# Kernel optimization log

Measured on AMD Instinct MI355X. Metric: run time of the kernel, lower is better.

## Reference

```python
import jax, jax.numpy as jnp
import numpy as np

T, D, H, E, K = 8192, 1024, 768, 16, 2


def setup_inputs() -> dict:
    key = jax.random.key(0)
    k1, k2, k3, k4, k5, k6 = jax.random.split(key, 6)
    x = jax.random.normal(k1, (T, D), dtype=jnp.float32)
    weights = jax.random.uniform(k2, (T, K), dtype=jnp.float32)
    indices = jax.random.randint(k3, (T, K), 0, E, dtype=jnp.int64)
    counts = jax.random.randint(k4, (E,), 0, 1024, dtype=jnp.int32)
    # GatedMLP params per expert: fc1: D -> 2H (value | gate), fc2: H -> D, no bias
    W1 = jax.random.normal(k5, (E, D, 2 * H), dtype=jnp.float32) * (1.0 / np.sqrt(D))
    W2 = jax.random.normal(k6, (E, H, D), dtype=jnp.float32) * (1.0 / np.sqrt(H))
    return {"x": x, "weights": weights, "indices": indices, "counts": counts, "W1": W1, "W2": W2}


def _gated_mlp(x, w1, w2):
    h = x @ w1                      # [T, 2H]
    v, g = jnp.split(h, 2, axis=-1)  # value, gate halves (torch chunk order)
    return (v * jax.nn.silu(g)) @ w2  # [T, D]


def reference(x, weights, indices, counts, W1, W2):
    # y[t] = sum_k weights[t,k] * GatedMLP_{indices[t,k]}(x[t])
    # Expressed as a masked per-expert combine: w_e[t] = sum_k weights[t,k]*[indices[t,k]==e].
    # Identical math to the torch gather/scatter loop (zero weight -> zero contribution).
    n_experts = W1.shape[0]
    y = jnp.zeros_like(x)
    for e in range(n_experts):
        w_e = jnp.sum(weights * (indices == e), axis=-1)  # [T]
        y = y + _gated_mlp(x, W1[e], W2[e]) * w_e[:, None]
    return y
```

## Files before the change

kernel.cpp:

```cpp
#include <hip/hip_runtime.h>
#include <hip/hip_bf16.h>

#define T_TOK 8192
#define D_DIM 1024
#define H_DIM 768
#define E_EXP 16
#define K_TOP 2
#define TK (T_TOK * K_TOP)
#define NT128 144

typedef __bf16 bf16x8 __attribute__((ext_vector_type(8)));
typedef unsigned short u16x8 __attribute__((ext_vector_type(8)));
typedef float f32x4 __attribute__((ext_vector_type(4)));

typedef const __attribute__((address_space(1))) void* gas_t;
typedef __attribute__((address_space(3))) void* las_t;

__device__ __forceinline__ unsigned short f2b(float f) {
    __hip_bfloat16 h = __float2bfloat16(f);
    return __builtin_bit_cast(unsigned short, h);
}
__device__ __forceinline__ float b2f(unsigned short u) {
    unsigned int x = ((unsigned int)u) << 16;
    return __builtin_bit_cast(float, x);
}

__global__ __launch_bounds__(1024) void k_route(
    const int* __restrict__ idx, const float* __restrict__ wts,
    int* __restrict__ offs, int* __restrict__ tiletab,
    int* __restrict__ rows, float* __restrict__ wslot, int* __restrict__ slot_of) {
    __shared__ int lcnt[E_EXP];
    __shared__ int lcur[E_EXP];
    const int tid = threadIdx.x;
    if (tid < E_EXP) lcnt[tid] = 0;
    __syncthreads();
    for (int i = tid; i < TK; i += 1024) atomicAdd(&lcnt[idx[i]], 1);
    __syncthreads();
    if (tid == 0) {
        int s = 0, nt = 0;
        for (int e = 0; e < E_EXP; ++e) {
            offs[e] = s;
            lcur[e] = s;
            const int n = lcnt[e];
            for (int m0 = 0; m0 < n; m0 += 128) tiletab[nt++] = (e << 16) | (m0 >> 7);
            s += n;
        }
        offs[E_EXP] = s;
        for (int i = nt; i < NT128; ++i) tiletab[i] = -1;
    }
    __syncthreads();
    for (int i = tid; i < TK; i += 1024) {
        const int e = idx[i];
        const int p = atomicAdd(&lcur[e], 1);
        rows[p] = i >> 1;
        wslot[p] = wts[i];
        slot_of[i] = p;
    }
}

#define PRB_X 2048
#define PRB_W1 3072
#define PRB_W2 1536
#define PRB_TOT (1 + PRB_X + PRB_W1 + PRB_W2)

__global__ __launch_bounds__(512) void k_preproute(
    const float* __restrict__ x, const float* __restrict__ W1, const float* __restrict__ W2,
    const int* __restrict__ idx, const float* __restrict__ wts,
    unsigned short* __restrict__ xb, unsigned short* __restrict__ W1T,
    unsigned short* __restrict__ W2T,
    int* __restrict__ offs, int* __restrict__ tiletab,
    int* __restrict__ rows, float* __restrict__ wslot, int* __restrict__ slot_of) {
    const int b = blockIdx.x;
    const int tid = threadIdx.x;
    if (b == 0) {
        __shared__ int lcnt[E_EXP];
        __shared__ int lcur[E_EXP];
        if (tid < E_EXP) lcnt[tid] = 0;
        __syncthreads();
        for (int i = tid; i < TK; i += 512) atomicAdd(&lcnt[idx[i]], 1);
        __syncthreads();
        if (tid == 0) {
            int s = 0, nt = 0;
            for (int e = 0; e < E_EXP; ++e) {
                offs[e] = s;
                lcur[e] = s;
                const int n = lcnt[e];
                for (int m0 = 0; m0 < n; m0 += 128) tiletab[nt++] = (e << 16) | (m0 >> 7);
                s += n;
            }
            offs[E_EXP] = s;
            for (int i = nt; i < NT128; ++i) tiletab[i] = -1;
        }
        __syncthreads();
        for (int i = tid; i < TK; i += 512) {
            const int e = idx[i];
            const int p = atomicAdd(&lcur[e], 1);
            rows[p] = i >> 1;
            wslot[p] = wts[i];
            slot_of[i] = p;
        }
        return;
    }
    if (b <= PRB_X) {
        const size_t base = (size_t)(b - 1) * 4096 + (size_t)tid * 8;
        const float4 v0 = *reinterpret_cast<const float4*>(&x[base]);
        const float4 v1 = *reinterpret_cast<const float4*>(&x[base + 4]);
        u16x8 u;
        u[0] = f2b(v0.x); u[1] = f2b(v0.y); u[2] = f2b(v0.z); u[3] = f2b(v0.w);
        u[4] = f2b(v1.x); u[5] = f2b(v1.y); u[6] = f2b(v1.z); u[7] = f2b(v1.w);
        *reinterpret_cast<u16x8*>(&xb[base]) = u;
        return;
    }
    __shared__ float t4[2][64][65];
    const int sub = tid >> 8, t2 = tid & 255;
    const float* src; unsigned short* dst;
    int K, C, e, kb, cb, pack;
    if (b <= PRB_X + PRB_W1) {
        const int q = (b - 1 - PRB_X) * 2 + sub;
        K = D_DIM; C = 2 * H_DIM; pack = 1;
        e = q / 384; const int r = q % 384;
        kb = (r % 16) * 64; cb = (r / 16) * 64;
        src = W1; dst = W1T;
    } else {
        const int q = (b - 1 - PRB_X - PRB_W1) * 2 + sub;
        K = H_DIM; C = D_DIM; pack = 0;
        e = q / 192; const int r = q % 192;
        kb = (r % 12) * 64; cb = (r / 12) * 64;
        src = W2; dst = W2T;
    }
    const float* s = src + ((size_t)e * K + kb) * C + cb;
#pragma unroll
    for (int i = 0; i < 4; ++i) {
        const int kk = (t2 >> 4) + i * 16, c4 = (t2 & 15) * 4;
        const float4 v = *reinterpret_cast<const float4*>(&s[(size_t)kk * C + c4]);
        t4[sub][kk][c4] = v.x; t4[sub][kk][c4 + 1] = v.y;
        t4[sub][kk][c4 + 2] = v.z; t4[sub][kk][c4 + 3] = v.w;
    }
    __syncthreads();
#pragma unroll
    for (int i = 0; i < 2; ++i) {
        const int cc = (t2 >> 3) + i * 32, k8 = (t2 & 7) * 8;
        const int j = cb + cc;
        int drow;
        if (pack) drow = (j < H_DIM) ? ((j >> 5) * 64 + (j & 31))
                                     : (((j - H_DIM) >> 5) * 64 + 32 + ((j - H_DIM) & 31));
        else drow = j;
        u16x8 u;
#pragma unroll
        for (int q8 = 0; q8 < 8; ++q8) u[q8] = f2b(t4[sub][k8 + q8][cc]);
        *reinterpret_cast<u16x8*>(&dst[((size_t)e * C + drow) * K + kb + k8]) = u;
    }
}


__global__ __launch_bounds__(512, 2) void k_gemm1_fast(
    const unsigned short* __restrict__ xb, const unsigned short* __restrict__ W1T,
    const int* __restrict__ offs, const int* __restrict__ tiletab,
    const int* __restrict__ rows, unsigned short* __restrict__ act) {
    const int ti = (blockIdx.x & 7) * (NT128 / 8) + (blockIdx.x >> 3);
    const int tt = tiletab[ti];
    if (tt < 0) return;
    const int e = tt >> 16, m0 = (tt & 0xffff) << 7;
    const int off = offs[e], n_e = offs[e + 1] - off;
    const int by = blockIdx.y;

    __shared__ unsigned short SA[2][128 * 32];
    __shared__ unsigned short SB[2][256 * 32];

    const int tid = threadIdx.x;
    const int wid = tid >> 6, lane = tid & 63;
    const int l15 = lane & 15, kq = lane >> 4;
    const int wm = wid >> 2, wn = wid & 3;
    const int srow = tid >> 2;
    const int esw = (((tid & 3) ^ ((tid >> 3) & 3)) << 3);
    const int rk = ((kq ^ ((l15 >> 1) & 3)) << 3);

    int tok;
    { int s = m0 + srow; s = (s < n_e) ? s : (n_e - 1); tok = rows[off + s]; }
    size_t bB[2];
#pragma unroll
    for (int j = 0; j < 2; ++j)
        bB[j] = ((size_t)e * (2 * H_DIM) + by * 256 + j * 128 + srow) * D_DIM + esw;

    f32x4 acc[4][4];
#pragma unroll
    for (int m = 0; m < 4; ++m)
#pragma unroll
        for (int n = 0; n < 4; ++n)
#pragma unroll
            for (int r = 0; r < 4; ++r) acc[m][n][r] = 0.f;

    auto stage = [&](int buf, int k0) {
        const unsigned short* ga = xb + (size_t)tok * D_DIM + k0 + esw;
        __builtin_amdgcn_global_load_lds((gas_t)ga,
            (las_t)((char*)&SA[buf][0] + tid * 16), 16, 0, 0);
#pragma unroll
        for (int j = 0; j < 2; ++j) {
            const unsigned short* gb = W1T + bB[j] + k0;
            __builtin_amdgcn_global_load_lds((gas_t)gb,
                (las_t)((char*)&SB[buf][0] + j * 8192 + tid * 16), 16, 0, 0);
        }
    };

    stage(0, 0);
    stage(1, 32);
    int c = 0;
    const int NT = D_DIM / 32;
    for (int t = 0; t < NT; ++t) {
        if (t < NT - 1) asm volatile("s_waitcnt vmcnt(3)" ::: "memory");
        else            asm volatile("s_waitcnt vmcnt(0)" ::: "memory");
        __builtin_amdgcn_s_barrier();
        asm volatile("" ::: "memory");
        bf16x8 a[4], b[4];
#pragma unroll
        for (int m = 0; m < 4; ++m) {
            const int row = wm * 64 + m * 16 + l15;
            a[m] = __builtin_bit_cast(bf16x8, *reinterpret_cast<const u16x8*>(
                &SA[c][row * 32 + rk]));
        }
#pragma unroll
        for (int n = 0; n < 4; ++n) {
            const int row = wn * 64 + n * 16 + l15;
            b[n] = __builtin_bit_cast(bf16x8, *reinterpret_cast<const u16x8*>(
                &SB[c][row * 32 + rk]));
        }
#pragma unroll
        for (int m = 0; m < 4; ++m)
#pragma unroll
            for (int n = 0; n < 4; ++n)
                acc[m][n] = __builtin_amdgcn_mfma_f32_16x16x32_bf16(a[m], b[n], acc[m][n], 0, 0, 0);
        asm volatile("s_waitcnt lgkmcnt(0)" ::: "memory");
        __builtin_amdgcn_s_barrier();
        asm volatile("" ::: "memory");
        if (t + 2 < NT) stage(c, (t + 2) * 32);
        c ^= 1;
    }
#pragma unroll
    for (int m = 0; m < 4; ++m)
#pragma unroll
        for (int r = 0; r < 4; ++r) {
            const int row = wm * 64 + m * 16 + kq * 4 + r;
            if (m0 + row < n_e) {
#pragma unroll
                for (int nv = 0; nv < 2; ++nv) {
                    const int col = by * 128 + wn * 32 + nv * 16 + l15;
                    const float vv = acc[m][nv][r], gg = acc[m][2 + nv][r];
                    const float s = gg / (1.0f + __expf(-gg));
                    act[(size_t)(off + m0 + row) * H_DIM + col] = f2b(vv * s);
                }
            }
        }
}

__global__ __launch_bounds__(512, 2) void k_gemm2_fast(
    const unsigned short* __restrict__ act, const unsigned short* __restrict__ W2T,
    const int* __restrict__ offs, const int* __restrict__ tiletab,
    const float* __restrict__ wslot, unsigned short* __restrict__ slot_out) {
    const int ti = (blockIdx.x & 7) * (NT128 / 8) + (blockIdx.x >> 3);
    const int tt = tiletab[ti];
    if (tt < 0) return;
    const int e = tt >> 16, m0 = (tt & 0xffff) << 7;
    const int off = offs[e], n_e = offs[e + 1] - off;
    const int by = blockIdx.y;

    __shared__ unsigned short SA[2][128 * 32];
    __shared__ unsigned short SB[2][256 * 32];

    const int tid = threadIdx.x;
    const int wid = tid >> 6, lane = tid & 63;
    const int l15 = lane & 15, kq = lane >> 4;
    const int wm = wid >> 2, wn = wid & 3;
    const int srow = tid >> 2;
    const int esw = (((tid & 3) ^ ((tid >> 3) & 3)) << 3);
    const int rk = ((kq ^ ((l15 >> 1) & 3)) << 3);

    int slotA;
    { int s = m0 + srow; s = (s < n_e) ? s : (n_e - 1); slotA = off + s; }
    size_t bB[2];
#pragma unroll
    for (int j = 0; j < 2; ++j)
        bB[j] = ((size_t)e * D_DIM + by * 256 + j * 128 + srow) * H_DIM + esw;

    f32x4 acc[4][4];
#pragma unroll
    for (int m = 0; m < 4; ++m)
#pragma unroll
        for (int n = 0; n < 4; ++n)
#pragma unroll
            for (int r = 0; r < 4; ++r) acc[m][n][r] = 0.f;

    auto stage = [&](int buf, int k0) {
        const unsigned short* ga = act + (size_t)slotA * H_DIM + k0 + esw;
        __builtin_amdgcn_global_load_lds((gas_t)ga,
            (las_t)((char*)&SA[buf][0] + tid * 16), 16, 0, 0);
#pragma unroll
        for (int j = 0; j < 2; ++j) {
            const unsigned short* gb = W2T + bB[j] + k0;
            __builtin_amdgcn_global_load_lds((gas_t)gb,
                (las_t)((char*)&SB[buf][0] + j * 8192 + tid * 16), 16, 0, 0);
        }
    };

    stage(0, 0);
    stage(1, 32);
    int c = 0;
    const int NT = H_DIM / 32;
    for (int t = 0; t < NT; ++t) {
        if (t < NT - 1) asm volatile("s_waitcnt vmcnt(3)" ::: "memory");
        else            asm volatile("s_waitcnt vmcnt(0)" ::: "memory");
        __builtin_amdgcn_s_barrier();
        asm volatile("" ::: "memory");
        bf16x8 a[4], b[4];
#pragma unroll
        for (int m = 0; m < 4; ++m) {
            const int row = wm * 64 + m * 16 + l15;
            a[m] = __builtin_bit_cast(bf16x8, *reinterpret_cast<const u16x8*>(
                &SA[c][row * 32 + rk]));
        }
#pragma unroll
        for (int n = 0; n < 4; ++n) {
            const int row = wn * 64 + n * 16 + l15;
            b[n] = __builtin_bit_cast(bf16x8, *reinterpret_cast<const u16x8*>(
                &SB[c][row * 32 + rk]));
        }
#pragma unroll
        for (int m = 0; m < 4; ++m)
#pragma unroll
            for (int n = 0; n < 4; ++n)
                acc[m][n] = __builtin_amdgcn_mfma_f32_16x16x32_bf16(a[m], b[n], acc[m][n], 0, 0, 0);
        asm volatile("s_waitcnt lgkmcnt(0)" ::: "memory");
        __builtin_amdgcn_s_barrier();
        asm volatile("" ::: "memory");
        if (t + 2 < NT) stage(c, (t + 2) * 32);
        c ^= 1;
    }
#pragma unroll
    for (int m = 0; m < 4; ++m)
#pragma unroll
        for (int r = 0; r < 4; ++r) {
            const int row = wm * 64 + m * 16 + kq * 4 + r;
            if (m0 + row < n_e) {
                const int slot = off + m0 + row;
                const float w = wslot[slot];
#pragma unroll
                for (int n = 0; n < 4; ++n) {
                    const int col = by * 256 + wn * 64 + n * 16 + l15;
                    slot_out[(size_t)slot * D_DIM + col] = f2b(w * acc[m][n][r]);
                }
            }
        }
}

__global__ __launch_bounds__(256) void k_gather(const float* __restrict__ x,
                                                const int* __restrict__ rows,
                                                unsigned short* __restrict__ xg) {
    const int s = blockIdx.x, t = threadIdx.x;
    const int tok = rows[s];
    const float4 v = *reinterpret_cast<const float4*>(&x[(size_t)tok * D_DIM + t * 4]);
    ushort4 u;
    u.x = f2b(v.x); u.y = f2b(v.y); u.z = f2b(v.z); u.w = f2b(v.w);
    *reinterpret_cast<ushort4*>(&xg[(size_t)s * D_DIM + t * 4]) = u;
}

__global__ __launch_bounds__(256) void k_gemm1_fb(
    const unsigned short* __restrict__ xg, const float* __restrict__ W1,
    const int* __restrict__ offs, const int* __restrict__ tiletab,
    unsigned short* __restrict__ act) {
    const int tt = tiletab[blockIdx.x];
    if (tt < 0) return;
    const int e = tt >> 16, m0 = (tt & 0xffff) << 7;
    const int off = offs[e], n_e = offs[e + 1] - off;
    const int h0 = blockIdx.y * 64;

    __shared__ unsigned short Ab[128 * 64];
    __shared__ unsigned short Bb[128 * 66];

    const int tid = threadIdx.x;
    const int wid = tid >> 6, lane = tid & 63;
    const int l15 = lane & 15, kq = lane >> 4;

    f32x4 acc[2][8];
#pragma unroll
    for (int m = 0; m < 2; ++m)
#pragma unroll
        for (int n = 0; n < 8; ++n)
#pragma unroll
            for (int r = 0; r < 4; ++r) acc[m][n][r] = 0.f;

    for (int k0 = 0; k0 < D_DIM; k0 += 64) {
        __syncthreads();
#pragma unroll
        for (int j = 0; j < 4; ++j) {
            const int o = wid * 4096 + j * 1024 + lane * 16;
            const int row = o >> 7, kb = o & 127;
            int gr = off + m0 + row; gr = (gr < TK) ? gr : (TK - 1);
            const unsigned short* gp = xg + (size_t)gr * D_DIM + k0 + (kb >> 1);
            __builtin_amdgcn_global_load_lds((gas_t)gp,
                (las_t)((char*)Ab + wid * 4096 + j * 1024), 16, 0, 0);
        }
        {
            const float* W1e = W1 + (size_t)e * D_DIM * (2 * H_DIM);
#pragma unroll
            for (int i = 0; i < 8; ++i) {
                const int flat = tid + 256 * i;
                const int cg = flat & 31, kk = flat >> 5;
                const int cc = cg * 4;
                const int gc = (cc < 64) ? (h0 + cc) : (H_DIM + h0 + cc - 64);
                const float4 v = *reinterpret_cast<const float4*>(
                    &W1e[(size_t)(k0 + kk) * (2 * H_DIM) + gc]);
                Bb[(cc + 0) * 66 + kk] = f2b(v.x);
                Bb[(cc + 1) * 66 + kk] = f2b(v.y);
                Bb[(cc + 2) * 66 + kk] = f2b(v.z);
                Bb[(cc + 3) * 66 + kk] = f2b(v.w);
            }
        }
        __syncthreads();
#pragma unroll
        for (int ks = 0; ks < 2; ++ks) {
            bf16x8 a[2], b[8];
#pragma unroll
            for (int m = 0; m < 2; ++m)
                a[m] = __builtin_bit_cast(bf16x8, *reinterpret_cast<const u16x8*>(
                    &Ab[(wid * 32 + m * 16 + l15) * 64 + ks * 32 + kq * 8]));
#pragma unroll
            for (int n = 0; n < 8; ++n)
                b[n] = __builtin_bit_cast(bf16x8, *reinterpret_cast<const u16x8*>(
                    &Bb[(n * 16 + l15) * 66 + ks * 32 + kq * 8]));
#pragma unroll
            for (int m = 0; m < 2; ++m)
#pragma unroll
                for (int n = 0; n < 8; ++n)
                    acc[m][n] = __builtin_amdgcn_mfma_f32_16x16x32_bf16(a[m], b[n], acc[m][n], 0, 0, 0);
        }
    }
#pragma unroll
    for (int m = 0; m < 2; ++m)
#pragma unroll
        for (int n = 0; n < 4; ++n)
#pragma unroll
            for (int r = 0; r < 4; ++r) {
                const int row = wid * 32 + m * 16 + kq * 4 + r;
                if (m0 + row < n_e) {
                    const float vv = acc[m][n][r], gg = acc[m][n + 4][r];
                    const float s = gg / (1.0f + __expf(-gg));
                    act[(size_t)(off + m0 + row) * H_DIM + h0 + n * 16 + l15] = f2b(vv * s);
                }
            }
}

__global__ __launch_bounds__(256) void k_gemm2_fb(
    const unsigned short* __restrict__ act, const float* __restrict__ W2,
    const int* __restrict__ offs, const int* __restrict__ tiletab,
    const float* __restrict__ wslot, unsigned short* __restrict__ slot_out,
    float* __restrict__ y, const int* __restrict__ rows, int atomic_mode) {
    const int tt = tiletab[blockIdx.x];
    if (tt < 0) return;
    const int e = tt >> 16, m0 = (tt & 0xffff) << 7;
    const int off = offs[e], n_e = offs[e + 1] - off;
    const int n0 = blockIdx.y * 64;

    __shared__ unsigned short Ab[128 * 64];
    __shared__ unsigned short Bb[64 * 66];

    const int tid = threadIdx.x;
    const int wid = tid >> 6, lane = tid & 63;
    const int l15 = lane & 15, kq = lane >> 4;

    f32x4 acc[2][4];
#pragma unroll
    for (int m = 0; m < 2; ++m)
#pragma unroll
        for (int n = 0; n < 4; ++n)
#pragma unroll
            for (int r = 0; r < 4; ++r) acc[m][n][r] = 0.f;

    for (int k0 = 0; k0 < H_DIM; k0 += 64) {
        __syncthreads();
#pragma unroll
        for (int j = 0; j < 4; ++j) {
            const int o = wid * 4096 + j * 1024 + lane * 16;
            const int row = o >> 7, kb = o & 127;
            int gr = off + m0 + row; gr = (gr < TK) ? gr : (TK - 1);
            const unsigned short* gp = act + (size_t)gr * H_DIM + k0 + (kb >> 1);
            __builtin_amdgcn_global_load_lds((gas_t)gp,
                (las_t)((char*)Ab + wid * 4096 + j * 1024), 16, 0, 0);
        }
        {
            const float* W2e = W2 + (size_t)e * H_DIM * D_DIM;
#pragma unroll
            for (int i = 0; i < 4; ++i) {
                const int flat = tid + 256 * i;
                const int cg = flat & 15, kk = flat >> 4;
                const int cc = cg * 4;
                const float4 v = *reinterpret_cast<const float4*>(
                    &W2e[(size_t)(k0 + kk) * D_DIM + n0 + cc]);
                Bb[(cc + 0) * 66 + kk] = f2b(v.x);
                Bb[(cc + 1) * 66 + kk] = f2b(v.y);
                Bb[(cc + 2) * 66 + kk] = f2b(v.z);
                Bb[(cc + 3) * 66 + kk] = f2b(v.w);
            }
        }
        __syncthreads();
#pragma unroll
        for (int ks = 0; ks < 2; ++ks) {
            bf16x8 a[2], b[4];
#pragma unroll
            for (int m = 0; m < 2; ++m)
                a[m] = __builtin_bit_cast(bf16x8, *reinterpret_cast<const u16x8*>(
                    &Ab[(wid * 32 + m * 16 + l15) * 64 + ks * 32 + kq * 8]));
#pragma unroll
            for (int n = 0; n < 4; ++n)
                b[n] = __builtin_bit_cast(bf16x8, *reinterpret_cast<const u16x8*>(
                    &Bb[(n * 16 + l15) * 66 + ks * 32 + kq * 8]));
#pragma unroll
            for (int m = 0; m < 2; ++m)
#pragma unroll
                for (int n = 0; n < 4; ++n)
                    acc[m][n] = __builtin_amdgcn_mfma_f32_16x16x32_bf16(a[m], b[n], acc[m][n], 0, 0, 0);
        }
    }
#pragma unroll
    for (int m = 0; m < 2; ++m)
#pragma unroll
        for (int r = 0; r < 4; ++r) {
            const int row = wid * 32 + m * 16 + kq * 4 + r;
            if (m0 + row < n_e) {
                const int slot = off + m0 + row;
                const float w = wslot[slot];
#pragma unroll
                for (int n = 0; n < 4; ++n) {
                    const float o = w * acc[m][n][r];
                    if (atomic_mode)
                        atomicAdd(&y[(size_t)rows[slot] * D_DIM + n0 + n * 16 + l15], o);
                    else
                        slot_out[(size_t)slot * D_DIM + n0 + n * 16 + l15] = f2b(o);
                }
            }
        }
}

__global__ __launch_bounds__(256) void k_combine(
    const unsigned short* __restrict__ slot_out, const int* __restrict__ slot_of,
    float* __restrict__ y) {
    const int t = blockIdx.x;
    const int d = threadIdx.x * 4;
    const int s0 = slot_of[2 * t], s1 = slot_of[2 * t + 1];
    const ushort4 a = *reinterpret_cast<const ushort4*>(&slot_out[(size_t)s0 * D_DIM + d]);
    const ushort4 b = *reinterpret_cast<const ushort4*>(&slot_out[(size_t)s1 * D_DIM + d]);
    float4 r;
    r.x = b2f(a.x) + b2f(b.x);
    r.y = b2f(a.y) + b2f(b.y);
    r.z = b2f(a.z) + b2f(b.z);
    r.w = b2f(a.w) + b2f(b.w);
    *reinterpret_cast<float4*>(&y[(size_t)t * D_DIM + d]) = r;
}

extern "C" void kernel_launch(void* const* d_in, const int* in_sizes, int n_in,
                              void* d_out, int out_size, void* d_ws, size_t ws_size,
                              hipStream_t stream) {
    const float* x = (const float*)d_in[0];
    const float* wts = (const float*)d_in[1];
    const int* idx = (const int*)d_in[2];
    const float* W1 = (const float*)d_in[4];
    const float* W2 = (const float*)d_in[5];
    float* y = (float*)d_out;

    char* ws = (char*)d_ws;
    int* offs = (int*)(ws + 128);
    int* tiletab = (int*)(ws + 320);
    int* rows = (int*)(ws + 2048);
    float* wslot = (float*)(ws + 2048 + (size_t)TK * 4);
    int* slot_of = (int*)(ws + 2048 + (size_t)TK * 8);
    const size_t OFF_XG = 2048 + (size_t)TK * 12;
    unsigned short* xg = (unsigned short*)(ws + OFF_XG);
    unsigned short* xb = xg;
    const size_t OFF_ACT = OFF_XG + (size_t)TK * D_DIM * 2;
    unsigned short* act = (unsigned short*)(ws + OFF_ACT);
    const size_t OFF_SO = OFF_ACT + (size_t)TK * H_DIM * 2;
    unsigned short* slot_out = (unsigned short*)(ws + OFF_SO);
    const size_t MID_END = OFF_SO + (size_t)TK * D_DIM * 2;
    const size_t OFF_W1T = MID_END;
    unsigned short* W1T = (unsigned short*)(ws + OFF_W1T);
    const size_t OFF_W2T = OFF_W1T + (size_t)E_EXP * 2 * H_DIM * D_DIM * 2;
    unsigned short* W2T = (unsigned short*)(ws + OFF_W2T);
    const size_t FULL_END = OFF_W2T + (size_t)E_EXP * D_DIM * H_DIM * 2;

    const int full = (ws_size >= FULL_END) ? 1 : 0;
    const int atomic_mode = (!full && ws_size < MID_END) ? 1 : 0;

    if (full) {
        k_preproute<<<PRB_TOT, 512, 0, stream>>>(x, W1, W2, idx, wts, xb, W1T, W2T,
                                                 offs, tiletab, rows, wslot, slot_of);
        dim3 g1(NT128, H_DIM / 128);
        k_gemm1_fast<<<g1, 512, 0, stream>>>(xb, W1T, offs, tiletab, rows, act);
        dim3 g2(NT128, D_DIM / 256);
        k_gemm2_fast<<<g2, 512, 0, stream>>>(act, W2T, offs, tiletab, wslot, slot_out);
        k_combine<<<T_TOK, 256, 0, stream>>>(slot_out, slot_of, y);
    } else {
        k_route<<<1, 1024, 0, stream>>>(idx, wts, offs, tiletab, rows, wslot, slot_of);
        k_gather<<<TK, 256, 0, stream>>>(x, rows, xg);
        dim3 g1(NT128, H_DIM / 64);
        k_gemm1_fb<<<g1, 256, 0, stream>>>(xg, W1, offs, tiletab, act);
        if (atomic_mode) hipMemsetAsync(y, 0, (size_t)out_size * 4, stream);
        dim3 g2(NT128, D_DIM / 64);
        k_gemm2_fb<<<g2, 256, 0, stream>>>(act, W2, offs, tiletab, wslot, slot_out, y, rows, atomic_mode);
        if (!atomic_mode)
            k_combine<<<T_TOK, 256, 0, stream>>>(slot_out, slot_of, y);
    }
}
```

Baseline: 208.9 us.

## Fuse MoE combine into GEMM2 via float atomics and use ballot-based routing

The second expert GEMM now scatters weighted results directly into the fp32 output with atomicAdd, after a memset. This removes the bf16 slot_out buffer and the separate combine kernel. Routing is rewritten to use wave ballots and popcounts in place of shared-memory atomics, which also makes slot order deterministic. In exchange, every output element takes two global float atomics, the memset adds work, and summation order becomes nondeterministic.

```diff
diff --git a/kernel.cpp b/kernel.cpp
--- a/kernel.cpp
+++ b/kernel.cpp
@@ -25,37 +25,71 @@
     return __builtin_bit_cast(float, x);
 }
 
-__global__ __launch_bounds__(1024) void k_route(
+__device__ __forceinline__ void route512(
     const int* __restrict__ idx, const float* __restrict__ wts,
     int* __restrict__ offs, int* __restrict__ tiletab,
     int* __restrict__ rows, float* __restrict__ wslot, int* __restrict__ slot_of) {
-    __shared__ int lcnt[E_EXP];
-    __shared__ int lcur[E_EXP];
+    __shared__ int wcnt[8][E_EXP];
+    __shared__ int wbase[8][E_EXP];
     const int tid = threadIdx.x;
-    if (tid < E_EXP) lcnt[tid] = 0;
-    __syncthreads();
-    for (int i = tid; i < TK; i += 1024) atomicAdd(&lcnt[idx[i]], 1);
+    const int w = tid >> 6, lane = tid & 63;
+    const unsigned long long ltmask = (1ull << lane) - 1ull;
+
+    int cnt[E_EXP];
+#pragma unroll
+    for (int e = 0; e < E_EXP; ++e) cnt[e] = 0;
+    for (int c = 0; c < 32; ++c) {
+        const int i = (w * 32 + c) * 64 + lane;
+        const int v = idx[i];
+#pragma unroll
+        for (int e = 0; e < E_EXP; ++e)
+            cnt[e] += (int)__popcll(__ballot(v == e));
+    }
+#pragma unroll
+    for (int e = 0; e < E_EXP; ++e)
+        if (lane == e) wcnt[w][e] = cnt[e];
     __syncthreads();
     if (tid == 0) {
         int s = 0, nt = 0;
         for (int e = 0; e < E_EXP; ++e) {
             offs[e] = s;
-            lcur[e] = s;
-            const int n = lcnt[e];
-            for (int m0 = 0; m0 < n; m0 += 128) tiletab[nt++] = (e << 16) | (m0 >> 7);
-            s += n;
+            int tot = 0;
+            for (int ww = 0; ww < 8; ++ww) { wbase[ww][e] = s + tot; tot += wcnt[ww][e]; }
+            for (int m0 = 0; m0 < tot; m0 += 128) tiletab[nt++] = (e << 16) | (m0 >> 7);
+            s += tot;
         }
         offs[E_EXP] = s;
-        for (int i = nt; i < NT128; ++i) tiletab[i] = -1;
+        for (int i2 = nt; i2 < NT128; ++i2) tiletab[i2] = -1;
     }
     __syncthreads();
-    for (int i = tid; i < TK; i += 1024) {
-        const int e = idx[i];
-        const int p = atomicAdd(&lcur[e], 1);
-        rows[p] = i >> 1;
-        wslot[p] = wts[i];
-        slot_of[i] = p;
-    }
+    int base[E_EXP];
+    {
+        int tmp = (lane < E_EXP) ? wbase[w][lane] : 0;
+#pragma unroll
+        for (int e = 0; e < E_EXP; ++e) base[e] = __shfl(tmp, e, 64);
+    }
+    for (int c = 0; c < 32; ++c) {
+        const int i = (w * 32 + c) * 64 + lane;
+        const int v = idx[i];
+        const float wt = wts[i];
+        int pos = 0;
+#pragma unroll
+        for (int e = 0; e < E_EXP; ++e) {
+            const unsigned long long mask = __ballot(v == e);
+            if (v == e) pos = base[e] + (int)__popcll(mask & ltmask);
+            base[e] += (int)__popcll(mask);
+        }
+        rows[pos] = i >> 1;
+        wslot[pos] = wt;
+        slot_of[i] = pos;
+    }
+}
+
+__global__ __launch_bounds__(512) void k_route(
+    const int* __restrict__ idx, const float* __restrict__ wts,
+    int* __restrict__ offs, int* __restrict__ tiletab,
+    int* __restrict__ rows, float* __restrict__ wslot, int* __restrict__ slot_of) {
+    route512(idx, wts, offs, tiletab, rows, wslot, slot_of);
 }
 
 #define PRB_X 2048
@@ -73,32 +107,7 @@
     const int b = blockIdx.x;
     const int tid = threadIdx.x;
     if (b == 0) {
-        __shared__ int lcnt[E_EXP];
-        __shared__ int lcur[E_EXP];
-        if (tid < E_EXP) lcnt[tid] = 0;
-        __syncthreads();
-        for (int i = tid; i < TK; i += 512) atomicAdd(&lcnt[idx[i]], 1);
-        __syncthreads();
-        if (tid == 0) {
-            int s = 0, nt = 0;
-            for (int e = 0; e < E_EXP; ++e) {
-                offs[e] = s;
-                lcur[e] = s;
-                const int n = lcnt[e];
-                for (int m0 = 0; m0 < n; m0 += 128) tiletab[nt++] = (e << 16) | (m0 >> 7);
-                s += n;
-            }
-            offs[E_EXP] = s;
-            for (int i = nt; i < NT128; ++i) tiletab[i] = -1;
-        }
-        __syncthreads();
-        for (int i = tid; i < TK; i += 512) {
-            const int e = idx[i];
-            const int p = atomicAdd(&lcur[e], 1);
-            rows[p] = i >> 1;
-            wslot[p] = wts[i];
-            slot_of[i] = p;
-        }
+        route512(idx, wts, offs, tiletab, rows, wslot, slot_of);
         return;
     }
     if (b <= PRB_X) {
@@ -255,7 +264,8 @@
 __global__ __launch_bounds__(512, 2) void k_gemm2_fast(
     const unsigned short* __restrict__ act, const unsigned short* __restrict__ W2T,
     const int* __restrict__ offs, const int* __restrict__ tiletab,
-    const float* __restrict__ wslot, unsigned short* __restrict__ slot_out) {
+    const float* __restrict__ wslot, const int* __restrict__ rows,
+    float* __restrict__ y) {
     const int ti = (blockIdx.x & 7) * (NT128 / 8) + (blockIdx.x >> 3);
     const int tt = tiletab[ti];
     if (tt < 0) return;
@@ -342,10 +352,11 @@
             if (m0 + row < n_e) {
                 const int slot = off + m0 + row;
                 const float w = wslot[slot];
+                const int tokr = rows[slot];
 #pragma unroll
                 for (int n = 0; n < 4; ++n) {
                     const int col = by * 256 + wn * 64 + n * 16 + l15;
-                    slot_out[(size_t)slot * D_DIM + col] = f2b(w * acc[m][n][r]);
+                    atomicAdd(&y[(size_t)tokr * D_DIM + col], w * acc[m][n][r]);
                 }
             }
         }
@@ -593,11 +604,11 @@
                                                  offs, tiletab, rows, wslot, slot_of);
         dim3 g1(NT128, H_DIM / 128);
         k_gemm1_fast<<<g1, 512, 0, stream>>>(xb, W1T, offs, tiletab, rows, act);
+        hipMemsetAsync(y, 0, (size_t)out_size * 4, stream);
         dim3 g2(NT128, D_DIM / 256);
-        k_gemm2_fast<<<g2, 512, 0, stream>>>(act, W2T, offs, tiletab, wslot, slot_out);
-        k_combine<<<T_TOK, 256, 0, stream>>>(slot_out, slot_of, y);
+        k_gemm2_fast<<<g2, 512, 0, stream>>>(act, W2T, offs, tiletab, wslot, rows, y);
     } else {
-        k_route<<<1, 1024, 0, stream>>>(idx, wts, offs, tiletab, rows, wslot, slot_of);
+        k_route<<<1, 512, 0, stream>>>(idx, wts, offs, tiletab, rows, wslot, slot_of);
         k_gather<<<TK, 256, 0, stream>>>(x, rows, xg);
         dim3 g1(NT128, H_DIM / 64);
         k_gemm1_fb<<<g1, 256, 0, stream>>>(xg, W1, offs, tiletab, act);
```

Measured after the change: 238.4 us. 1.14x slower.
